# Kernel tuning notes

Measured on AMD Instinct MI355X. Metric: run time of the kernel, lower is better.

## Reference

```python
import jax, jax.numpy as jnp
import numpy as np

B, N, S, C, H = 16, 64, 4096, 768, 1
HEAD_DIM = C // H
SCALE = HEAD_DIM ** -0.5
ASSIGN_EPS = 1.0


def setup_inputs() -> dict:
    key = jax.random.key(0)
    ks = jax.random.split(key, 8)
    w = lambda k: jax.random.normal(k, (C, C), jnp.float32) * 0.02
    return {
        "query": jax.random.normal(ks[0], (B, N, C), jnp.float32),       # group tokens
        "key_tokens": jax.random.normal(ks[1], (B, S, C), jnp.float32),  # sequence tokens
        "Wq": w(ks[2]), "bq": jnp.zeros((C,), jnp.float32),
        "Wk": w(ks[3]), "bk": jnp.zeros((C,), jnp.float32),
        "Wv": w(ks[4]), "bv": jnp.zeros((C,), jnp.float32),
        "Wo": w(ks[5]), "bo": jnp.zeros((C,), jnp.float32),
    }


def reference(query, key_tokens, Wq, bq, Wk, bk, Wv, bv, Wo, bo):
    # AssignAttention forward (hard=True, gumbel=False -> hard_softmax path).
    def split_heads(x):  # [b, t, C] -> [b, h, t, c]
        b, t, _ = x.shape
        return x.reshape(b, t, H, HEAD_DIM).transpose(0, 2, 1, 3)

    q = split_heads(query @ Wq.T + bq)        # [B, H, N, c]
    k = split_heads(key_tokens @ Wk.T + bk)   # [B, H, S, c]
    v = split_heads(key_tokens @ Wv.T + bv)   # [B, H, S, c]

    raw_attn = jnp.einsum('bhnc,bhsc->bhns', q, k) * SCALE  # [B, H, N, S]

    # hard_softmax over the group (query) dim, axis=-2, with straight-through estimator
    y_soft = jax.nn.softmax(raw_attn, axis=-2)
    idx = jnp.argmax(y_soft, axis=-2)                          # [B, H, S]
    y_hard = jnp.swapaxes(jax.nn.one_hot(idx, N, dtype=raw_attn.dtype), -1, -2)  # [B, H, N, S]
    attn = jax.lax.stop_gradient(y_hard - y_soft) + y_soft

    # sum-renormalization over assigned tokens (sum_assign=False)
    attn = attn / (attn.sum(axis=-1, keepdims=True) + ASSIGN_EPS)

    out = jnp.einsum('bhns,bhsc->bhnc', attn, v)  # [B, H, N, c]
    out = out.transpose(0, 2, 1, 3).reshape(B, N, C)
    return out @ Wo.T + bo
```

## Files before the change

kernel.cpp:

```cpp
#include <hip/hip_runtime.h>
#include <hip/hip_bf16.h>

#define BQ 16
#define NG 64
#define SQ 4096
#define CD 768
#define ROWS (BQ*NG)

template<bool TRANSB, int BIAS_MODE>
__global__ __launch_bounds__(256)
void gemm_k768(const float* __restrict__ A, const float* __restrict__ B,
               const float* __restrict__ bias, const int* __restrict__ cnt,
               float* __restrict__ outp)
{
    __shared__ float At[64][65];
    __shared__ float Bt[64][65];
    const int tid  = threadIdx.x;
    const int r0   = blockIdx.y * 64;
    const int c0   = blockIdx.x * 64;
    const int rg   = tid & 15;
    const int cg   = tid >> 4;
    const int lrow = tid >> 4;
    const int c4   = tid & 15;

    float  accC[4][4];
    double acc64[4][4];
#pragma unroll
    for (int i = 0; i < 4; ++i)
#pragma unroll
        for (int j = 0; j < 4; ++j) { accC[i][j] = 0.f; acc64[i][j] = 0.0; }

    for (int kc = 0; kc < CD; kc += 64) {
#pragma unroll
        for (int p = 0; p < 4; ++p) {
            const int row = p * 16 + lrow;
            const float4 v = *(const float4*)(A + (size_t)(r0 + row) * CD + kc + 4 * c4);
            At[row][4*c4+0] = v.x; At[row][4*c4+1] = v.y;
            At[row][4*c4+2] = v.z; At[row][4*c4+3] = v.w;
        }
#pragma unroll
        for (int p = 0; p < 4; ++p) {
            const int row = p * 16 + lrow;
            const float4 v = TRANSB
                ? *(const float4*)(B + (size_t)(c0 + row) * CD + kc + 4 * c4)
                : *(const float4*)(B + (size_t)(kc + row) * CD + c0 + 4 * c4);
            Bt[row][4*c4+0] = v.x; Bt[row][4*c4+1] = v.y;
            Bt[row][4*c4+2] = v.z; Bt[row][4*c4+3] = v.w;
        }
        __syncthreads();
#pragma unroll 4
        for (int dd = 0; dd < 64; ++dd) {
            float a[4], b[4];
#pragma unroll
            for (int i = 0; i < 4; ++i) a[i] = At[4*rg + i][dd];
#pragma unroll
            for (int j = 0; j < 4; ++j)
                b[j] = TRANSB ? Bt[4*cg + j][dd] : Bt[dd][4*cg + j];
#pragma unroll
            for (int i = 0; i < 4; ++i)
#pragma unroll
                for (int j = 0; j < 4; ++j) accC[i][j] += a[i] * b[j];
        }
        __syncthreads();
#pragma unroll
        for (int i = 0; i < 4; ++i)
#pragma unroll
            for (int j = 0; j < 4; ++j) { acc64[i][j] += (double)accC[i][j]; accC[i][j] = 0.f; }
    }

#pragma unroll
    for (int i = 0; i < 4; ++i) {
        const int r = r0 + 4 * rg + i;
        float invf = 1.f, bsc = 0.f;
        if (BIAS_MODE == 2) {
            const int cv = cnt[r];
            invf = 1.f / ((float)cv + 1.f);
            bsc  = (float)cv * invf;
        }
#pragma unroll
        for (int j = 0; j < 4; ++j) {
            const int c = c0 + 4 * cg + j;
            float v = (float)acc64[i][j];
            if (BIAS_MODE == 1)      v += bias[c];
            else if (BIAS_MODE == 2) v = v * invf + bsc * bias[c];
            outp[(size_t)r * CD + c] = v;
        }
    }
}

__global__ __launch_bounds__(256)
void row_dot_bk(const float* __restrict__ q, const float* __restrict__ bk,
                double* __restrict__ delta)
{
    const int r    = blockIdx.x * 4 + (threadIdx.x >> 6);
    const int lane = threadIdx.x & 63;
    double acc = 0.0;
    for (int c = lane; c < CD; c += 64)
        acc += (double)q[(size_t)r * CD + c] * (double)bk[c];
    for (int off = 32; off; off >>= 1) acc += __shfl_down(acc, off, 64);
    if (lane == 0) delta[r] = acc;
}

struct ScoreTiles { float gt[64][68]; float kt[64][132]; };
struct ScoreRed   { double bval[128][17]; int bidx[128][17]; };
union  ScoreShared { ScoreTiles t; ScoreRed r; };

__global__ __launch_bounds__(256)
void score_argmax(const float* __restrict__ g, const float* __restrict__ key,
                  const double* __restrict__ delta, int* __restrict__ idxo)
{
    __shared__ alignas(16) ScoreShared sh;
    __shared__ double dl[64];
    const int tid  = threadIdx.x;
    const int b    = blockIdx.y;
    const int s0   = blockIdx.x * 128;
    const int sg   = tid & 15;
    const int ng   = tid >> 4;
    const int lrow = tid >> 4;
    const int c4   = tid & 15;

    if (tid < 64) dl[tid] = delta[b * 64 + tid];

    float  accC[4][8];
    double acc64[4][8];
#pragma unroll
    for (int i = 0; i < 4; ++i)
#pragma unroll
        for (int j = 0; j < 8; ++j) { accC[i][j] = 0.f; acc64[i][j] = 0.0; }

    for (int kc = 0; kc < CD; kc += 64) {
#pragma unroll
        for (int p = 0; p < 4; ++p) {
            const int nrow = p * 16 + lrow;
            const float4 v = *(const float4*)(g + (size_t)(b * 64 + nrow) * CD + kc + 4 * c4);
            sh.t.gt[4*c4+0][nrow] = v.x; sh.t.gt[4*c4+1][nrow] = v.y;
            sh.t.gt[4*c4+2][nrow] = v.z; sh.t.gt[4*c4+3][nrow] = v.w;
        }
#pragma unroll
        for (int p = 0; p < 8; ++p) {
            const int srow = p * 16 + lrow;
            const float4 v = *(const float4*)(key + (size_t)(b * SQ + s0 + srow) * CD + kc + 4 * c4);
            sh.t.kt[4*c4+0][srow] = v.x; sh.t.kt[4*c4+1][srow] = v.y;
            sh.t.kt[4*c4+2][srow] = v.z; sh.t.kt[4*c4+3][srow] = v.w;
        }
        __syncthreads();
#pragma unroll 4
        for (int dd = 0; dd < 64; ++dd) {
            const float4 ga = *(const float4*)&sh.t.gt[dd][4 * ng];
            const float4 k0 = *(const float4*)&sh.t.kt[dd][8 * sg];
            const float4 k1 = *(const float4*)&sh.t.kt[dd][8 * sg + 4];
            const float gs[4] = { ga.x, ga.y, ga.z, ga.w };
            const float ks[8] = { k0.x, k0.y, k0.z, k0.w, k1.x, k1.y, k1.z, k1.w };
#pragma unroll
            for (int i = 0; i < 4; ++i)
#pragma unroll
                for (int j = 0; j < 8; ++j) accC[i][j] += gs[i] * ks[j];
        }
        __syncthreads();
#pragma unroll
        for (int i = 0; i < 4; ++i)
#pragma unroll
            for (int j = 0; j < 8; ++j) { acc64[i][j] += (double)accC[i][j]; accC[i][j] = 0.f; }
    }

    double bv[8]; int bn[8];
#pragma unroll
    for (int j = 0; j < 8; ++j) {
        bv[j] = acc64[0][j] + dl[4 * ng + 0]; bn[j] = 4 * ng + 0;
#pragma unroll
        for (int i = 1; i < 4; ++i) {
            const double v = acc64[i][j] + dl[4 * ng + i];
            if (v > bv[j]) { bv[j] = v; bn[j] = 4 * ng + i; }
        }
    }
    __syncthreads();
#pragma unroll
    for (int j = 0; j < 8; ++j) {
        sh.r.bval[8 * sg + j][ng] = bv[j];
        sh.r.bidx[8 * sg + j][ng] = bn[j];
    }
    __syncthreads();
    if (tid < 128) {
        const int s = tid;
        double best = sh.r.bval[s][0]; int bi = sh.r.bidx[s][0];
        for (int k = 1; k < 16; ++k) {
            const double v = sh.r.bval[s][k];
            if (v > best) { best = v; bi = sh.r.bidx[s][k]; }
        }
        idxo[b * SQ + s0 + s] = bi;
    }
}

__global__ __launch_bounds__(256)
void gather_ksum(const float* __restrict__ key, const int* __restrict__ idx,
                 float* __restrict__ Ksum, int* __restrict__ cnt)
{
    __shared__ int slist[SQ];
    __shared__ int scount;
    const int n   = blockIdx.x;
    const int b   = blockIdx.y;
    const int tid = threadIdx.x;
    if (tid == 0) scount = 0;
    __syncthreads();

    const int* ib = idx + b * SQ;
#pragma unroll
    for (int p = 0; p < SQ / 256; ++p) {
        const int s = p * 256 + tid;
        if (ib[s] == n) {
            const int pos = atomicAdd(&scount, 1);
            slist[pos] = s;
        }
    }
    __syncthreads();
    const int m = scount;

    double a0 = 0.0, a1 = 0.0, a2 = 0.0;
    const float* kb = key + (size_t)b * SQ * CD;
    const int c1 = tid + 256, c2 = tid + 512;

    int r = 0;
    for (; r + 4 <= m; r += 4) {
        const int s0 = slist[r], s1 = slist[r + 1], s2 = slist[r + 2], s3 = slist[r + 3];
        const float* p0 = kb + (size_t)s0 * CD;
        const float* p1 = kb + (size_t)s1 * CD;
        const float* p2 = kb + (size_t)s2 * CD;
        const float* p3 = kb + (size_t)s3 * CD;
        const float v00 = p0[tid], v01 = p0[c1], v02 = p0[c2];
        const float v10 = p1[tid], v11 = p1[c1], v12 = p1[c2];
        const float v20 = p2[tid], v21 = p2[c1], v22 = p2[c2];
        const float v30 = p3[tid], v31 = p3[c1], v32 = p3[c2];
        a0 += (double)v00 + (double)v10 + (double)v20 + (double)v30;
        a1 += (double)v01 + (double)v11 + (double)v21 + (double)v31;
        a2 += (double)v02 + (double)v12 + (double)v22 + (double)v32;
    }
    for (; r < m; ++r) {
        const float* p0 = kb + (size_t)slist[r] * CD;
        a0 += (double)p0[tid]; a1 += (double)p0[c1]; a2 += (double)p0[c2];
    }

    float* out = Ksum + (size_t)(b * 64 + n) * CD;
    out[tid] = (float)a0; out[c1] = (float)a1; out[c2] = (float)a2;
    if (tid == 0) cnt[b * 64 + n] = m;
}

extern "C" void kernel_launch(void* const* d_in, const int* in_sizes, int n_in,
                              void* d_out, int out_size, void* d_ws, size_t ws_size,
                              hipStream_t stream)
{
    const float* query = (const float*)d_in[0];
    const float* key   = (const float*)d_in[1];
    const float* Wq    = (const float*)d_in[2];
    const float* bq    = (const float*)d_in[3];
    const float* Wk    = (const float*)d_in[4];
    const float* bk    = (const float*)d_in[5];
    const float* Wv    = (const float*)d_in[6];
    const float* bv    = (const float*)d_in[7];
    const float* Wo    = (const float*)d_in[8];
    const float* bo    = (const float*)d_in[9];

    char* ws = (char*)d_ws;
    int*    cnt   = (int*)   (ws + 0);
    float*  Ksum  = (float*) (ws + 4096);
    double* delta = (double*)(ws + 3149824);
    float*  q     = (float*) (ws + 3158016);
    float*  g     = (float*) (ws + 6303744);
    float*  T1    = (float*) (ws + 9449472);
    int*    idx   = (int*)   (ws + 12595200);

    const dim3 gg(CD / 64, ROWS / 64);

    gemm_k768<true, 1><<<gg, 256, 0, stream>>>(query, Wq, bq, nullptr, q);
    row_dot_bk<<<ROWS / 4, 256, 0, stream>>>(q, bk, delta);
    gemm_k768<false, 0><<<gg, 256, 0, stream>>>(q, Wk, nullptr, nullptr, g);
    score_argmax<<<dim3(SQ / 128, BQ), 256, 0, stream>>>(g, key, delta, idx);
    gather_ksum<<<dim3(NG, BQ), 256, 0, stream>>>(key, idx, Ksum, cnt);
    gemm_k768<true, 2><<<gg, 256, 0, stream>>>(Ksum, Wv, bv, cnt, T1);
    gemm_k768<true, 1><<<gg, 256, 0, stream>>>(T1, Wo, bo, nullptr, (float*)d_out);
}
```

Before: 613.1 us.

## Fold projection weights into fused Wq·Wk and Wv·Wo products with split-K GEMMs

Precomputes combined weight matrices Wq^T·Wk and Wv^T·Wo^T, together with the matching bias vectors, so that each activation needs only one GEMM instead of two. All GEMMs are replaced by a split-K kernel with 8x8 register tiles, followed by a separate fp64 reduction pass that applies the bias and count normalisation. This removes the per-tile fp64 accumulation and one GEMM on each side. In exchange it adds transposes, weight-product GEMMs on every call, and extra global traffic for the partial sums.

```diff
diff --git a/kernel.cpp b/kernel.cpp
--- a/kernel.cpp
+++ b/kernel.cpp
@@ -6,99 +6,130 @@
 #define SQ 4096
 #define CD 768
 #define ROWS (BQ*NG)
-
-template<bool TRANSB, int BIAS_MODE>
-__global__ __launch_bounds__(256)
-void gemm_k768(const float* __restrict__ A, const float* __restrict__ B,
-               const float* __restrict__ bias, const int* __restrict__ cnt,
-               float* __restrict__ outp)
-{
-    __shared__ float At[64][65];
-    __shared__ float Bt[64][65];
-    const int tid  = threadIdx.x;
-    const int r0   = blockIdx.y * 64;
-    const int c0   = blockIdx.x * 64;
-    const int rg   = tid & 15;
-    const int cg   = tid >> 4;
-    const int lrow = tid >> 4;
-    const int c4   = tid & 15;
-
-    float  accC[4][4];
-    double acc64[4][4];
-#pragma unroll
-    for (int i = 0; i < 4; ++i)
-#pragma unroll
-        for (int j = 0; j < 4; ++j) { accC[i][j] = 0.f; acc64[i][j] = 0.0; }
-
-    for (int kc = 0; kc < CD; kc += 64) {
-#pragma unroll
-        for (int p = 0; p < 4; ++p) {
-            const int row = p * 16 + lrow;
-            const float4 v = *(const float4*)(A + (size_t)(r0 + row) * CD + kc + 4 * c4);
-            At[row][4*c4+0] = v.x; At[row][4*c4+1] = v.y;
-            At[row][4*c4+2] = v.z; At[row][4*c4+3] = v.w;
-        }
-#pragma unroll
-        for (int p = 0; p < 4; ++p) {
-            const int row = p * 16 + lrow;
-            const float4 v = TRANSB
-                ? *(const float4*)(B + (size_t)(c0 + row) * CD + kc + 4 * c4)
-                : *(const float4*)(B + (size_t)(kc + row) * CD + c0 + 4 * c4);
-            Bt[row][4*c4+0] = v.x; Bt[row][4*c4+1] = v.y;
-            Bt[row][4*c4+2] = v.z; Bt[row][4*c4+3] = v.w;
-        }
-        __syncthreads();
-#pragma unroll 4
-        for (int dd = 0; dd < 64; ++dd) {
-            float a[4], b[4];
-#pragma unroll
-            for (int i = 0; i < 4; ++i) a[i] = At[4*rg + i][dd];
-#pragma unroll
-            for (int j = 0; j < 4; ++j)
-                b[j] = TRANSB ? Bt[4*cg + j][dd] : Bt[dd][4*cg + j];
-#pragma unroll
-            for (int i = 0; i < 4; ++i)
-#pragma unroll
-                for (int j = 0; j < 4; ++j) accC[i][j] += a[i] * b[j];
-        }
-        __syncthreads();
-#pragma unroll
-        for (int i = 0; i < 4; ++i)
-#pragma unroll
-            for (int j = 0; j < 4; ++j) { acc64[i][j] += (double)accC[i][j]; accC[i][j] = 0.f; }
-    }
-
-#pragma unroll
-    for (int i = 0; i < 4; ++i) {
-        const int r = r0 + 4 * rg + i;
-        float invf = 1.f, bsc = 0.f;
-        if (BIAS_MODE == 2) {
-            const int cv = cnt[r];
-            invf = 1.f / ((float)cv + 1.f);
-            bsc  = (float)cv * invf;
-        }
-#pragma unroll
-        for (int j = 0; j < 4; ++j) {
-            const int c = c0 + 4 * cg + j;
-            float v = (float)acc64[i][j];
-            if (BIAS_MODE == 1)      v += bias[c];
-            else if (BIAS_MODE == 2) v = v * invf + bsc * bias[c];
-            outp[(size_t)r * CD + c] = v;
-        }
-    }
-}
-
-__global__ __launch_bounds__(256)
-void row_dot_bk(const float* __restrict__ q, const float* __restrict__ bk,
-                double* __restrict__ delta)
+#define KS 12
+
+__global__ __launch_bounds__(256)
+void transpose64(const float* __restrict__ src, float* __restrict__ dst,
+                 int M, int N)
+{
+    __shared__ float t[64][65];
+    const int bx = blockIdx.x * 64;
+    const int by = blockIdx.y * 64;
+    const int tx = threadIdx.x & 63, tw = threadIdx.x >> 6;
+#pragma unroll
+    for (int i = 0; i < 16; ++i) {
+        const int row = i * 4 + tw;
+        t[row][tx] = src[(size_t)(by + row) * N + bx + tx];
+    }
+    __syncthreads();
+#pragma unroll
+    for (int i = 0; i < 16; ++i) {
+        const int row = i * 4 + tw;
+        dst[(size_t)(bx + row) * M + by + tx] = t[tx][row];
+    }
+}
+
+__global__ __launch_bounds__(256)
+void vecmatT(const float* __restrict__ Mm, const float* __restrict__ v,
+             float* __restrict__ out)
+{
+    __shared__ float red[4][64];
+    const int j0 = blockIdx.x * 64;
+    const int jl = threadIdx.x & 63;
+    const int cs = threadIdx.x >> 6;
+    double a = 0.0;
+    for (int c = cs; c < CD; c += 4)
+        a += (double)Mm[(size_t)c * CD + j0 + jl] * (double)v[c];
+    red[cs][jl] = (float)a;
+    __syncthreads();
+    if (cs == 0) out[j0 + jl] = red[0][jl] + red[1][jl] + red[2][jl] + red[3][jl];
+}
+
+__global__ __launch_bounds__(256)
+void delta_q(const float* __restrict__ query, const float* __restrict__ uq,
+             const float* __restrict__ bq, const float* __restrict__ bk,
+             double* __restrict__ delta)
 {
     const int r    = blockIdx.x * 4 + (threadIdx.x >> 6);
     const int lane = threadIdx.x & 63;
-    double acc = 0.0;
-    for (int c = lane; c < CD; c += 64)
-        acc += (double)q[(size_t)r * CD + c] * (double)bk[c];
-    for (int off = 32; off; off >>= 1) acc += __shfl_down(acc, off, 64);
-    if (lane == 0) delta[r] = acc;
+    double a = 0.0, b = 0.0;
+    for (int c = lane; c < CD; c += 64) {
+        a += (double)query[(size_t)r * CD + c] * (double)uq[c];
+        b += (double)bq[c] * (double)bk[c];
+    }
+    a += b;
+    for (int off = 32; off; off >>= 1) a += __shfl_down(a, off, 64);
+    if (lane == 0) delta[r] = a;
+}
+
+__global__ __launch_bounds__(64)
+void gemm64sk(const float* __restrict__ AT, int lda,
+              const float* __restrict__ B, int ldb,
+              float* __restrict__ P, int M)
+{
+    __shared__ float As[64][68];
+    __shared__ float Bs[64][68];
+    const int lane = threadIdx.x;
+    const int c0 = blockIdx.x * 64, r0 = blockIdx.y * 64, k0 = blockIdx.z * 64;
+    const int q4 = lane & 15, qr = lane >> 4;
+#pragma unroll
+    for (int i = 0; i < 16; ++i) {
+        const int kk = i * 4 + qr;
+        *(float4*)&As[kk][4 * q4] = *(const float4*)(AT + (size_t)(k0 + kk) * lda + r0 + 4 * q4);
+        *(float4*)&Bs[kk][4 * q4] = *(const float4*)(B  + (size_t)(k0 + kk) * ldb + c0 + 4 * q4);
+    }
+    __syncthreads();
+    const int rg = lane & 7, cg = lane >> 3;
+    float acc[8][8];
+#pragma unroll
+    for (int i = 0; i < 8; ++i)
+#pragma unroll
+        for (int j = 0; j < 8; ++j) acc[i][j] = 0.f;
+
+#pragma unroll 2
+    for (int dd = 0; dd < 64; ++dd) {
+        const float4 a0 = *(const float4*)&As[dd][8 * rg];
+        const float4 a1 = *(const float4*)&As[dd][8 * rg + 4];
+        const float4 b0 = *(const float4*)&Bs[dd][8 * cg];
+        const float4 b1 = *(const float4*)&Bs[dd][8 * cg + 4];
+        const float av[8] = {a0.x, a0.y, a0.z, a0.w, a1.x, a1.y, a1.z, a1.w};
+        const float bv[8] = {b0.x, b0.y, b0.z, b0.w, b1.x, b1.y, b1.z, b1.w};
+#pragma unroll
+        for (int i = 0; i < 8; ++i)
+#pragma unroll
+            for (int j = 0; j < 8; ++j) acc[i][j] += av[i] * bv[j];
+    }
+    float* Pz = P + (size_t)blockIdx.z * M * CD;
+#pragma unroll
+    for (int i = 0; i < 8; ++i) {
+        const int r = r0 + 8 * rg + i;
+        float4 v0; v0.x = acc[i][0]; v0.y = acc[i][1]; v0.z = acc[i][2]; v0.w = acc[i][3];
+        float4 v1; v1.x = acc[i][4]; v1.y = acc[i][5]; v1.z = acc[i][6]; v1.w = acc[i][7];
+        *(float4*)(Pz + (size_t)r * CD + c0 + 8 * cg)     = v0;
+        *(float4*)(Pz + (size_t)r * CD + c0 + 8 * cg + 4) = v1;
+    }
+}
+
+__global__ __launch_bounds__(256)
+void reduce_sk(const float* __restrict__ P, const float* __restrict__ bias,
+               const float* __restrict__ bias2, const int* __restrict__ cnt,
+               float* __restrict__ out, int M, int mode)
+{
+    const int e = blockIdx.x * 256 + threadIdx.x;
+    if (e >= M * CD) return;
+    const size_t MN = (size_t)M * CD;
+    double a = 0.0;
+#pragma unroll
+    for (int z = 0; z < KS; ++z) a += (double)P[z * MN + e];
+    float v = (float)a;
+    if (mode == 1) v += bias[e % CD];
+    else if (mode == 3) {
+        const int r = e / CD;
+        const int cv = cnt[r];
+        const float invf = 1.f / ((float)cv + 1.f);
+        v = v * invf + ((float)cv * invf) * bias2[e % CD] + bias[e % CD];
+    }
+    out[e] = v;
 }
 
 struct ScoreTiles { float gt[64][68]; float kt[64][132]; };
@@ -226,13 +257,9 @@
         const float* p1 = kb + (size_t)s1 * CD;
         const float* p2 = kb + (size_t)s2 * CD;
         const float* p3 = kb + (size_t)s3 * CD;
-        const float v00 = p0[tid], v01 = p0[c1], v02 = p0[c2];
-        const float v10 = p1[tid], v11 = p1[c1], v12 = p1[c2];
-        const float v20 = p2[tid], v21 = p2[c1], v22 = p2[c2];
-        const float v30 = p3[tid], v31 = p3[c1], v32 = p3[c2];
-        a0 += (double)v00 + (double)v10 + (double)v20 + (double)v30;
-        a1 += (double)v01 + (double)v11 + (double)v21 + (double)v31;
-        a2 += (double)v02 + (double)v12 + (double)v22 + (double)v32;
+        a0 += (double)p0[tid] + (double)p1[tid] + (double)p2[tid] + (double)p3[tid];
+        a1 += (double)p0[c1] + (double)p1[c1] + (double)p2[c1] + (double)p3[c1];
+        a2 += (double)p0[c2] + (double)p1[c2] + (double)p2[c2] + (double)p3[c2];
     }
     for (; r < m; ++r) {
         const float* p0 = kb + (size_t)slist[r] * CD;
@@ -260,21 +287,38 @@
     const float* bo    = (const float*)d_in[9];
 
     char* ws = (char*)d_ws;
+    const size_t MB = 1 << 20;
     int*    cnt   = (int*)   (ws + 0);
-    float*  Ksum  = (float*) (ws + 4096);
-    double* delta = (double*)(ws + 3149824);
-    float*  q     = (float*) (ws + 3158016);
-    float*  g     = (float*) (ws + 6303744);
-    float*  T1    = (float*) (ws + 9449472);
-    int*    idx   = (int*)   (ws + 12595200);
-
-    const dim3 gg(CD / 64, ROWS / 64);
-
-    gemm_k768<true, 1><<<gg, 256, 0, stream>>>(query, Wq, bq, nullptr, q);
-    row_dot_bk<<<ROWS / 4, 256, 0, stream>>>(q, bk, delta);
-    gemm_k768<false, 0><<<gg, 256, 0, stream>>>(q, Wk, nullptr, nullptr, g);
+    double* delta = (double*)(ws + 4096);
+    float*  uq    = (float*) (ws + 16384);
+    float*  bqk   = (float*) (ws + 19456);
+    float*  bvo   = (float*) (ws + 22528);
+    int*    idx   = (int*)   (ws + 32768);
+    float*  qT    = (float*) (ws + 1 * MB);
+    float*  WoT   = (float*) (ws + 4 * MB);
+    float*  Wqk   = (float*) (ws + 7 * MB);
+    float*  g     = (float*) (ws + 10 * MB);
+    float*  Wvo   = (float*) (ws + 13 * MB);
+    float*  Ksum  = (float*) (ws + 16 * MB);
+    float*  KsumT = (float*) (ws + 20 * MB);
+    float*  P     = (float*) (ws + 24 * MB);
+
+    transpose64<<<dim3(12, 12), 256, 0, stream>>>(Wo, WoT, CD, CD);
+    vecmatT<<<12, 256, 0, stream>>>(Wq, bk, uq);
+    vecmatT<<<12, 256, 0, stream>>>(Wk, bq, bqk);
+    vecmatT<<<12, 256, 0, stream>>>(WoT, bv, bvo);
+    gemm64sk<<<dim3(12, 12, KS), 64, 0, stream>>>(Wq, CD, Wk, CD, P, CD);
+    reduce_sk<<<2304, 256, 0, stream>>>(P, nullptr, nullptr, nullptr, Wqk, CD, 0);
+    gemm64sk<<<dim3(12, 12, KS), 64, 0, stream>>>(Wv, CD, WoT, CD, P, CD);
+    reduce_sk<<<2304, 256, 0, stream>>>(P, nullptr, nullptr, nullptr, Wvo, CD, 0);
+
+    transpose64<<<dim3(12, 16), 256, 0, stream>>>(query, qT, ROWS, CD);
+    delta_q<<<ROWS / 4, 256, 0, stream>>>(query, uq, bq, bk, delta);
+    gemm64sk<<<dim3(12, 16, KS), 64, 0, stream>>>(qT, ROWS, Wqk, CD, P, ROWS);
+    reduce_sk<<<3072, 256, 0, stream>>>(P, bqk, nullptr, nullptr, g, ROWS, 1);
     score_argmax<<<dim3(SQ / 128, BQ), 256, 0, stream>>>(g, key, delta, idx);
     gather_ksum<<<dim3(NG, BQ), 256, 0, stream>>>(key, idx, Ksum, cnt);
-    gemm_k768<true, 2><<<gg, 256, 0, stream>>>(Ksum, Wv, bv, cnt, T1);
-    gemm_k768<true, 1><<<gg, 256, 0, stream>>>(T1, Wo, bo, nullptr, (float*)d_out);
-}
+    transpose64<<<dim3(12, 16), 256, 0, stream>>>(Ksum, KsumT, ROWS, CD);
+    gemm64sk<<<dim3(12, 16, KS), 64, 0, stream>>>(KsumT, ROWS, Wvo, CD, P, ROWS);
+    reduce_sk<<<3072, 256, 0, stream>>>(P, bo, bvo, cnt, (float*)d_out, ROWS, 3);
+}
```

Result: slower. 767.4 us (+25.2%).
